# Kernel optimization log

Measured on AMD Instinct MI355X. Metric: run time of the kernel, lower is better.

## Reference

```python
import jax, jax.numpy as jnp
import numpy as np
from math import pi

N = 20000        # nodes
E = 640000       # edges (avg degree 32)
H = 128          # hidden_channels = num_filters
NB = 3           # num_bond_features
NGS = 50 - NB    # gaussians in smearing (num_gaussians - num_bond_features)
CUT = 10.0       # cutoff
L = 3            # num_interactions
B = 16           # graphs in batch
LOG2 = 0.6931471805599453


def ssp(x):
    # ShiftedSoftplus
    return jax.nn.softplus(x) - LOG2


def setup_inputs() -> dict:
    key = jax.random.key(0)
    ks = jax.random.split(key, 20)
    s = 0.05
    inp = {
        "z": jax.random.randint(ks[0], (N,), 0, 100),
        "pos": jax.random.uniform(ks[1], (N, 3), jnp.float32),
        "batch": jnp.sort(jax.random.randint(ks[2], (N,), 0, B)),
        "edge_index": jax.random.randint(ks[3], (2, E), 0, N),
        "edge_attr": jax.random.uniform(ks[4], (E, NB), jnp.float32),
        # parameters (stacked over L interaction blocks where per-layer)
        "emb": jax.random.normal(ks[5], (100, H), jnp.float32) * s,
        "mlp_w1": jax.random.normal(ks[6], (L, NB + NGS, H), jnp.float32) * s,
        "mlp_b1": jnp.zeros((L, H), jnp.float32),
        "mlp_w2": jax.random.normal(ks[7], (L, H, H), jnp.float32) * s,
        "mlp_b2": jnp.zeros((L, H), jnp.float32),
        "cf1_w": jax.random.normal(ks[8], (L, H, H), jnp.float32) * s,   # lin1, no bias
        "cf2_w": jax.random.normal(ks[9], (L, H, H), jnp.float32) * s,
        "cf2_b": jnp.zeros((L, H), jnp.float32),
        "lin_w": jax.random.normal(ks[10], (L, H, H), jnp.float32) * s,
        "lin_b": jnp.zeros((L, H), jnp.float32),
        "out1_w": jax.random.normal(ks[11], (H, H // 2), jnp.float32) * s,
        "out1_b": jnp.zeros((H // 2,), jnp.float32),
        "out2_w": jax.random.normal(ks[12], (H // 2, 1), jnp.float32) * s,
        "out2_b": jnp.zeros((1,), jnp.float32),
    }
    return inp


def reference(z, pos, batch, edge_index, edge_attr, emb,
              mlp_w1, mlp_b1, mlp_w2, mlp_b2,
              cf1_w, cf2_w, cf2_b, lin_w, lin_b,
              out1_w, out1_b, out2_w, out2_b):
    row, col = edge_index[0], edge_index[1]  # source j, target i
    h = emb[z]                               # [N,H] embedding_e(z)
    # edge_weight = ||pos[row] - pos[col]||
    ew = jnp.linalg.norm(pos[row] - pos[col], axis=-1)  # [E]
    # GaussianSmearing(0, cutoff, NGS)
    offset = jnp.linspace(0.0, CUT, NGS, dtype=jnp.float32)
    coeff = -0.5 / (offset[1] - offset[0]) ** 2
    gs = jnp.exp(coeff * (ew[:, None] - offset[None, :]) ** 2)  # [E,NGS]
    ea = jnp.concatenate([edge_attr, gs], axis=1)  # [E,50]
    # cosine cutoff weight
    C = 0.5 * (jnp.cos(ew * pi / CUT) + 1.0)       # [E]
    for l in range(L):
        # filter MLP on edge features
        W = ssp(ea @ mlp_w1[l] + mlp_b1[l]) @ mlp_w2[l] + mlp_b2[l]  # [E,H]
        W = W * C[:, None]
        xh = h @ cf1_w[l]                    # lin1 (no bias) [N,H]
        msg = xh[row] * W                    # gather-mul [E,H]
        agg = jax.ops.segment_sum(msg, col, num_segments=N)  # scatter-add [N,H]
        xc = agg @ cf2_w[l] + cf2_b[l]       # lin2
        xc = ssp(xc)
        xc = xc @ lin_w[l] + lin_b[l]        # block output lin
        h = h + xc                           # residual
    h = ssp(h @ out1_w + out1_b)             # [N,H/2]
    per_node = h @ out2_w + out2_b           # [N,1]
    out = jax.ops.segment_sum(per_node, batch, num_segments=B)  # readout 'add' -> [B,1]
    return out
```

## Files before the change

### kernel.cpp

```cpp
#include <hip/hip_runtime.h>
#include <hip/hip_bf16.h>

typedef __attribute__((ext_vector_type(8))) short bfrag;
typedef __attribute__((ext_vector_type(4))) float f32x4;

__device__ __forceinline__ float ssp_f(float x) {
    return fmaxf(x, 0.f) + __logf(1.f + __expf(-fabsf(x))) - 0.6931471805599453f;
}

__device__ __forceinline__ unsigned short f2b(float x) {
    __hip_bfloat16 h = __float2bfloat16(x);
    return *(unsigned short*)&h;
}

__device__ __forceinline__ unsigned int pk2(float a, float b) {
    __hip_bfloat162 h2 = __float22bfloat162_rn(make_float2(a, b));
    return *(unsigned int*)&h2;
}

__device__ __forceinline__ void stage32x128(
    const float* __restrict__ src, long r0, int N, int t, short (*dst)[136])
{
    #pragma unroll
    for (int j = 0; j < 4; ++j) {
        const int fi = t + j * 256;
        const int r = fi >> 5, c4 = (fi & 31) << 2;
        const long n = r0 + r;
        float4 v = make_float4(0.f, 0.f, 0.f, 0.f);
        if (n < N) v = *(const float4*)(src + n * 128 + c4);
        *(uint2*)&dst[r][c4] = make_uint2(pk2(v.x, v.y), pk2(v.z, v.w));
    }
}

__global__ void sniff_kernel(const unsigned int* __restrict__ raw, int* __restrict__ flag)
{
    __shared__ int cnt[256];
    const int t = threadIdx.x;
    unsigned int w = raw[t];
    unsigned int e = (w >> 7) & 0xFFu;
    cnt[t] = (e >= 100u && e <= 135u) ? 1 : 0;
    __syncthreads();
    for (int s = 128; s > 0; s >>= 1) {
        if (t < s) cnt[t] += cnt[t + s];
        __syncthreads();
    }
    if (t == 0) *flag = (cnt[0] >= 160) ? 1 : 0;
}

__global__ void sniff_int_kernel(const unsigned int* __restrict__ z, int* __restrict__ iflag)
{
    __shared__ int cnt[128];
    const int t = threadIdx.x;
    cnt[t] = (z[2 * t + 1] == 0u) ? 1 : 0;
    __syncthreads();
    for (int s = 64; s > 0; s >>= 1) {
        if (t < s) cnt[t] += cnt[t + s];
        __syncthreads();
    }
    if (t == 0) *iflag = (cnt[0] >= 126) ? 1 : 0;
}

struct Cvt16 {
    const void* src[16];
    long off[17];
};

__global__ __launch_bounds__(256) void convert_fused_kernel(
    Cvt16 args, float* __restrict__ F, long total, const int* __restrict__ flag)
{
    long i = (long)blockIdx.x * 256 + threadIdx.x;
    if (i >= total) return;
    int lo = 0, hi = 16;
    while (hi - lo > 1) {
        int mid = (lo + hi) >> 1;
        if (i >= args.off[mid]) lo = mid; else hi = mid;
    }
    long loc = i - args.off[lo];
    if (*flag) F[i] = __bfloat162float(((const __hip_bfloat16*)args.src[lo])[loc]);
    else       F[i] = ((const float*)args.src[lo])[loc];
}

__global__ __launch_bounds__(256) void convert_int_kernel(
    const void* __restrict__ src, int* __restrict__ dst, int n,
    const int* __restrict__ iflag)
{
    int i = blockIdx.x * 256 + threadIdx.x;
    if (i >= n) return;
    if (*iflag) dst[i] = (int)(((const long long*)src)[i]);
    else        dst[i] = ((const int*)src)[i];
}

__global__ __launch_bounds__(256) void embed_kernel(
    const int* __restrict__ z, const float* __restrict__ embf,
    float* __restrict__ h, int NH)
{
    int idx = blockIdx.x * 256 + threadIdx.x;
    if (idx >= NH) return;
    h[idx] = embf[z[idx >> 7] * 128 + (idx & 127)];
}

__global__ __launch_bounds__(256) void zero_int_kernel(int* p, int n)
{
    int i = blockIdx.x * 256 + threadIdx.x;
    if (i < n) p[i] = 0;
}

__global__ __launch_bounds__(256) void hist_kernel(const int* __restrict__ col,
                                                   int* __restrict__ count, int E)
{
    int e = blockIdx.x * 256 + threadIdx.x;
    if (e < E) atomicAdd(&count[col[e]], 1);
}

__global__ __launch_bounds__(256) void scan_kernel(const int* __restrict__ count,
                                                   int* __restrict__ rowptr,
                                                   int* __restrict__ next, int N)
{
    __shared__ int part[256];
    const int t = threadIdx.x;
    const int chunk = (N + 255) / 256;
    const int lo = t * chunk, hi = min(lo + chunk, N);
    int s = 0;
    for (int i = lo; i < hi; ++i) s += count[i];
    part[t] = s;
    __syncthreads();
    if (t == 0) {
        int run = 0;
        for (int i = 0; i < 256; ++i) { int v = part[i]; part[i] = run; run += v; }
        rowptr[N] = run;
    }
    __syncthreads();
    int run = part[t];
    for (int i = lo; i < hi; ++i) {
        rowptr[i] = run; next[i] = run;
        run += count[i];
    }
}

__global__ __launch_bounds__(256) void prep_scatter_kernel(
    const float* __restrict__ posf, const int* __restrict__ row,
    const int* __restrict__ col, const float* __restrict__ eattrf,
    int* __restrict__ next,
    int* __restrict__ rowS, int* __restrict__ colS,
    float* __restrict__ CS, float* __restrict__ ewS,
    unsigned short* __restrict__ eaS, int E, int NB)
{
    int e = blockIdx.x * 256 + threadIdx.x;
    if (e >= E) return;
    const int r = row[e], c = col[e];
    const int p = atomicAdd(&next[c], 1);
    float dx = posf[r*3+0] - posf[c*3+0];
    float dy = posf[r*3+1] - posf[c*3+1];
    float dz = posf[r*3+2] - posf[c*3+2];
    float ew = sqrtf(dx*dx + dy*dy + dz*dz);
    rowS[p] = r; colS[p] = c; ewS[p] = ew;
    CS[p] = 0.5f * (cosf(ew * 0.3141592653589793f) + 1.0f);
    unsigned short* o = eaS + (long)p * 4;
    for (int q = 0; q < 4; ++q)
        o[q] = (q < NB) ? f2b(eattrf[(long)e * NB + q]) : (unsigned short)0;
}

__global__ __launch_bounds__(256) void wtrans_kernel(
    const float* __restrict__ src, unsigned short* __restrict__ dst,
    int K, int Kpad, int N)
{
    int idx = blockIdx.x * 256 + threadIdx.x;
    if (idx >= N * Kpad) return;
    int n = idx / Kpad, k = idx - n * Kpad;
    dst[idx] = (k < K) ? f2b(src[k * N + n]) : (unsigned short)0;
}

__global__ __launch_bounds__(256) void wtrans_node_kernel(
    const float* __restrict__ cf1, const float* __restrict__ cf2,
    const float* __restrict__ lin, unsigned short* __restrict__ dst, int total)
{
    int idx = blockIdx.x * 256 + threadIdx.x;
    if (idx >= total) return;
    int m = idx >> 14;
    int fam = m % 3, l = m / 3;
    int local = idx & 16383;
    int n = local >> 7, k = local & 127;
    const float* src = (fam == 0 ? cf1 : fam == 1 ? cf2 : lin) + (long)l * 16384;
    dst[idx] = f2b(src[k * 128 + n]);
}

template<int MODE>
__global__ __launch_bounds__(256) void node_gemm_tiled(
    const float* __restrict__ in, const float* __restrict__ W,
    const float* __restrict__ bias, float* __restrict__ out, int N)
{
    __shared__ float in_s[32][128];
    const int t = threadIdx.x;
    const long n0 = (long)blockIdx.x * 32;
    for (int i = t; i < 32 * 128; i += 256) {
        long n = n0 + (i >> 7);
        in_s[i >> 7][i & 127] = (n < N) ? in[n * 128 + (i & 127)] : 0.f;
    }
    __syncthreads();
    const int j = t & 31, sub = t >> 5;
    const int c4 = j * 4, rb = sub * 4;
    float acc[4][4];
    float4 bv = make_float4(0.f, 0.f, 0.f, 0.f);
    if (MODE != 0) bv = *(const float4*)(bias + c4);
    #pragma unroll
    for (int i = 0; i < 4; ++i) { acc[i][0]=bv.x; acc[i][1]=bv.y; acc[i][2]=bv.z; acc[i][3]=bv.w; }
    #pragma unroll 4
    for (int k = 0; k < 128; ++k) {
        const float4 wv = *(const float4*)(W + k * 128 + c4);
        #pragma unroll
        for (int i = 0; i < 4; ++i) {
            const float a = in_s[rb + i][k];
            acc[i][0] += a * wv.x; acc[i][1] += a * wv.y;
            acc[i][2] += a * wv.z; acc[i][3] += a * wv.w;
        }
    }
    #pragma unroll
    for (int i = 0; i < 4; ++i) {
        long n = n0 + rb + i;
        if (n >= N) continue;
        float4 o;
        if (MODE == 1) {
            o.x = ssp_f(acc[i][0]); o.y = ssp_f(acc[i][1]);
            o.z = ssp_f(acc[i][2]); o.w = ssp_f(acc[i][3]);
        } else {
            o.x = acc[i][0]; o.y = acc[i][1]; o.z = acc[i][2]; o.w = acc[i][3];
        }
        if (MODE == 2) {
            float4 p = *(const float4*)(out + n * 128 + c4);
            o.x += p.x; o.y += p.y; o.z += p.z; o.w += p.w;
        }
        *(float4*)(out + n * 128 + c4) = o;
    }
}

__global__ __launch_bounds__(256) void node_gemm1_mfma(
    const float* __restrict__ in, const unsigned short* __restrict__ wt,
    float* __restrict__ out, float* __restrict__ aggz, int N)
{
    __shared__ __align__(16) short a_b[32][136];
    const int t = threadIdx.x;
    const long r0 = (long)blockIdx.x * 32;
    stage32x128(in, r0, N, t, a_b);
    {
        const float4 z = make_float4(0.f, 0.f, 0.f, 0.f);
        #pragma unroll
        for (int j = 0; j < 4; ++j) {
            const int fi = t + j * 256;
            const long n = r0 + (fi >> 5);
            if (n < N) *(float4*)(aggz + n * 128 + ((fi & 31) << 2)) = z;
        }
    }
    __syncthreads();
    const int lane = t & 63, w = t >> 6;
    const int colL = lane & 15, quad = lane >> 4;
    const int rt = (w & 1) * 16 + colL;
    const int nh = (w >> 1) * 64;
    f32x4 acc[4];
    #pragma unroll
    for (int tt = 0; tt < 4; ++tt) acc[tt] = (f32x4){0.f, 0.f, 0.f, 0.f};
    #pragma unroll
    for (int ks = 0; ks < 4; ++ks) {
        const bfrag a = *(const bfrag*)&a_b[rt][ks * 32 + quad * 8];
        #pragma unroll
        for (int tt = 0; tt < 4; ++tt) {
            const bfrag wf = *(const bfrag*)&wt[(long)(nh + tt * 16 + colL) * 128 + ks * 32 + quad * 8];
            acc[tt] = __builtin_amdgcn_mfma_f32_16x16x32_bf16(wf, a, acc[tt], 0, 0, 0);
        }
    }
    const long node = r0 + rt;
    if (node < N) {
        float* orow = out + node * 128;
        #pragma unroll
        for (int tt = 0; tt < 4; ++tt) {
            const int c0 = nh + tt * 16 + quad * 4;
            *(float4*)(orow + c0) = make_float4(acc[tt][0], acc[tt][1], acc[tt][2], acc[tt][3]);
        }
    }
}

__global__ __launch_bounds__(256) void node_gemm23_mfma(
    const float* __restrict__ in,
    const unsigned short* __restrict__ w1t, const float* __restrict__ b1,
    const unsigned short* __restrict__ w2t, const float* __restrict__ b2,
    float* __restrict__ h, int N)
{
    __shared__ __align__(16) short a_b[32][136];
    __shared__ __align__(16) short t_b[32][136];
    const int t = threadIdx.x;
    const long r0 = (long)blockIdx.x * 32;
    stage32x128(in, r0, N, t, a_b);
    __syncthreads();
    const int lane = t & 63, w = t >> 6;
    const int colL = lane & 15, quad = lane >> 4;
    const int rt = (w & 1) * 16 + colL;
    const int nh = (w >> 1) * 64;
    {
        f32x4 acc[4];
        #pragma unroll
        for (int tt = 0; tt < 4; ++tt) acc[tt] = (f32x4){0.f, 0.f, 0.f, 0.f};
        #pragma unroll
        for (int ks = 0; ks < 4; ++ks) {
            const bfrag a = *(const bfrag*)&a_b[rt][ks * 32 + quad * 8];
            #pragma unroll
            for (int tt = 0; tt < 4; ++tt) {
                const bfrag wf = *(const bfrag*)&w1t[(long)(nh + tt * 16 + colL) * 128 + ks * 32 + quad * 8];
                acc[tt] = __builtin_amdgcn_mfma_f32_16x16x32_bf16(wf, a, acc[tt], 0, 0, 0);
            }
        }
        #pragma unroll
        for (int tt = 0; tt < 4; ++tt) {
            const int c0 = nh + tt * 16 + quad * 4;
            const float4 bv = *(const float4*)(b1 + c0);
            const float v0 = ssp_f(acc[tt][0] + bv.x);
            const float v1 = ssp_f(acc[tt][1] + bv.y);
            const float v2 = ssp_f(acc[tt][2] + bv.z);
            const float v3 = ssp_f(acc[tt][3] + bv.w);
            *(uint2*)&t_b[rt][c0] = make_uint2(pk2(v0, v1), pk2(v2, v3));
        }
    }
    __syncthreads();
    {
        f32x4 acc[4];
        #pragma unroll
        for (int tt = 0; tt < 4; ++tt) acc[tt] = (f32x4){0.f, 0.f, 0.f, 0.f};
        #pragma unroll
        for (int ks = 0; ks < 4; ++ks) {
            const bfrag a = *(const bfrag*)&t_b[rt][ks * 32 + quad * 8];
            #pragma unroll
            for (int tt = 0; tt < 4; ++tt) {
                const bfrag wf = *(const bfrag*)&w2t[(long)(nh + tt * 16 + colL) * 128 + ks * 32 + quad * 8];
                acc[tt] = __builtin_amdgcn_mfma_f32_16x16x32_bf16(wf, a, acc[tt], 0, 0, 0);
            }
        }
        const long node = r0 + rt;
        if (node < N) {
            float* hrow = h + node * 128;
            #pragma unroll
            for (int tt = 0; tt < 4; ++tt) {
                const int c0 = nh + tt * 16 + quad * 4;
                const float4 bv = *(const float4*)(b2 + c0);
                float4 hv = *(const float4*)(hrow + c0);
                hv.x += acc[tt][0] + bv.x;
                hv.y += acc[tt][1] + bv.y;
                hv.z += acc[tt][2] + bv.z;
                hv.w += acc[tt][3] + bv.w;
                *(float4*)(hrow + c0) = hv;
            }
        }
    }
}

__global__ __launch_bounds__(256, 8) void edge_mfma(
    const int* __restrict__ rowS, const int* __restrict__ colS,
    const float* __restrict__ CS, const float* __restrict__ ewS,
    const unsigned short* __restrict__ eaS,
    const unsigned short* __restrict__ w1t, const float* __restrict__ b1,
    const unsigned short* __restrict__ w2t, const float* __restrict__ b2,
    const float* __restrict__ xh, float* __restrict__ agg,
    int E, int NB, int F50, float delta, float coeff)
{
    __shared__ __align__(16) char smem[32 * 132 * 4];
    short (*ea_b)[64]    = (short(*)[64])smem;
    short (*t_b)[128]    = (short(*)[128])(smem + 4096);
    float (*runbuf)[132] = (float(*)[132])smem;
    __shared__ int   row_s[32];
    __shared__ int   col_s[32];
    __shared__ float C_s[32];
    __shared__ float ew_s[32];

    const int t = threadIdx.x;
    const long p0 = (long)blockIdx.x * 32;

    if (t < 32) {
        long p = p0 + t; if (p >= E) p = E - 1;
        row_s[t] = rowS[p];
        col_s[t] = colS[p];
        C_s[t]   = (p0 + t < E) ? CS[p] : 0.f;
        ew_s[t]  = ewS[p];
    }
    __syncthreads();
    #pragma unroll
    for (int j = 0; j < 4; ++j) {
        const int pi = t + j * 256;
        const int e  = pi >> 5;
        const int k0 = (pi & 31) * 2;
        long p = p0 + e; if (p >= E) p = E - 1;
        const float ew = ew_s[e];
        float f[2];
        #pragma unroll
        for (int q = 0; q < 2; ++q) {
            const int k = k0 + q;
            if (k < NB) {
                unsigned int ui = (unsigned int)eaS[p * 4 + k] << 16;
                f[q] = *(float*)&ui;
            } else if (k < F50) {
                const float d = ew - (float)(k - NB) * delta;
                f[q] = __expf(coeff * d * d);
            } else f[q] = 0.f;
        }
        *(unsigned int*)&ea_b[e][k0 ^ ((e & 7) << 3)] = pk2(f[0], f[1]);
    }
    __syncthreads();

    const int lane = t & 63;
    const int w    = t >> 6;
    const int colL = lane & 15;
    const int quad = lane >> 4;
    const int et   = (w & 1) * 16 + colL;
    const int nh   = (w >> 1) * 64;
    const int esw  = (et & 7) << 3;
    const float Ct = C_s[et];

    {
        f32x4 acc[4];
        #pragma unroll
        for (int tt = 0; tt < 4; ++tt) acc[tt] = (f32x4){0.f, 0.f, 0.f, 0.f};
        #pragma unroll
        for (int ks = 0; ks < 2; ++ks) {
            const bfrag ea = *(const bfrag*)&ea_b[et][(ks * 32 + quad * 8) ^ esw];
            #pragma unroll
            for (int tt = 0; tt < 4; ++tt) {
                const bfrag wf = *(const bfrag*)&w1t[(long)(nh + tt * 16 + colL) * 64 + ks * 32 + quad * 8];
                acc[tt] = __builtin_amdgcn_mfma_f32_16x16x32_bf16(wf, ea, acc[tt], 0, 0, 0);
            }
        }
        #pragma unroll
        for (int tt = 0; tt < 4; ++tt) {
            const int c0 = nh + tt * 16 + quad * 4;
            const float4 bv = *(const float4*)(b1 + c0);
            const float v0 = ssp_f(acc[tt][0] + bv.x) * Ct;
            const float v1 = ssp_f(acc[tt][1] + bv.y) * Ct;
            const float v2 = ssp_f(acc[tt][2] + bv.z) * Ct;
            const float v3 = ssp_f(acc[tt][3] + bv.w) * Ct;
            *(uint2*)&t_b[et][c0 ^ esw] = make_uint2(pk2(v0, v1), pk2(v2, v3));
        }
    }
    __syncthreads();

    {
        const float* xrow = xh + (long)row_s[et] * 128;
        const float4 xv0 = *(const float4*)(xrow + nh +  0 + quad * 4);
        const float4 xv1 = *(const float4*)(xrow + nh + 16 + quad * 4);
        const float4 xv2 = *(const float4*)(xrow + nh + 32 + quad * 4);
        const float4 xv3 = *(const float4*)(xrow + nh + 48 + quad * 4);
        f32x4 acc[4];
        #pragma unroll
        for (int tt = 0; tt < 4; ++tt) acc[tt] = (f32x4){0.f, 0.f, 0.f, 0.f};
        #pragma unroll
        for (int ks = 0; ks < 4; ++ks) {
            const bfrag tf = *(const bfrag*)&t_b[et][(ks * 32 + quad * 8) ^ esw];
            #pragma unroll
            for (int tt = 0; tt < 4; ++tt) {
                const bfrag wf = *(const bfrag*)&w2t[(long)(nh + tt * 16 + colL) * 128 + ks * 32 + quad * 8];
                acc[tt] = __builtin_amdgcn_mfma_f32_16x16x32_bf16(wf, tf, acc[tt], 0, 0, 0);
            }
        }
        __syncthreads();
        const float4 xv[4] = {xv0, xv1, xv2, xv3};
        #pragma unroll
        for (int tt = 0; tt < 4; ++tt) {
            const int c0 = nh + tt * 16 + quad * 4;
            const float4 bv = *(const float4*)(b2 + c0);
            float4 o;
            o.x = (acc[tt][0] + Ct * bv.x) * xv[tt].x;
            o.y = (acc[tt][1] + Ct * bv.y) * xv[tt].y;
            o.z = (acc[tt][2] + Ct * bv.z) * xv[tt].z;
            o.w = (acc[tt][3] + Ct * bv.w) * xv[tt].w;
            *(float4*)&runbuf[et][c0] = o;
        }
    }
    __syncthreads();

    {
        const int cc   = t & 127;
        const int e0h  = (t >> 7) * 16;
        float a     = runbuf[e0h][cc];
        int  curcol = col_s[e0h];
        #pragma unroll 4
        for (int e = e0h + 1; e < e0h + 16; ++e) {
            const int c2 = col_s[e];
            if (c2 != curcol) {
                atomicAdd(&agg[(long)curcol * 128 + cc], a);
                a = 0.f; curcol = c2;
            }
            a += runbuf[e][cc];
        }
        atomicAdd(&agg[(long)curcol * 128 + cc], a);
    }
}

__global__ __launch_bounds__(256) void edge_atomic(
    const float* __restrict__ posf,
    const int* __restrict__ row, const int* __restrict__ col,
    const float* __restrict__ eattrf,
    const float* __restrict__ w1, const float* __restrict__ b1,
    const float* __restrict__ w2, const float* __restrict__ b2,
    const float* __restrict__ xh, float* __restrict__ agg,
    int E, int NB, int F50, float delta, float coeff)
{
    __shared__ float ea_s[32][52];
    __shared__ float t_s[32][128];
    __shared__ int   row_s[32];
    __shared__ int   col_s[32];
    __shared__ float C_s[32];
    __shared__ float ew_s[32];

    const int t = threadIdx.x;
    const long e0 = (long)blockIdx.x * 32;

    if (t < 32) {
        long e = e0 + t; if (e >= E) e = E - 1;
        const int r = row[e], c = col[e];
        row_s[t] = r; col_s[t] = c;
        float dx = posf[r*3+0] - posf[c*3+0];
        float dy = posf[r*3+1] - posf[c*3+1];
        float dz = posf[r*3+2] - posf[c*3+2];
        float ew = sqrtf(dx*dx + dy*dy + dz*dz);
        ew_s[t] = ew;
        C_s[t]  = (e0 + t < E) ? 0.5f * (cosf(ew * 0.3141592653589793f) + 1.0f) : 0.f;
        for (int q = 0; q < NB; ++q)
            ea_s[t][q] = eattrf[e * NB + q];
    }
    __syncthreads();
    {
        const int NGS = F50 - NB;
        for (int i = t; i < 32 * NGS; i += 256) {
            const int e = i / NGS, g = i - e * NGS;
            const float d = ew_s[e] - (float)g * delta;
            ea_s[e][NB + g] = __expf(coeff * d * d);
        }
    }
    __syncthreads();

    const int j = t & 31, sub = t >> 5;
    const int c4 = j * 4, eb = sub * 4;
    float acc[4][4];
    {
        const float4 bv = *(const float4*)(b1 + c4);
        #pragma unroll
        for (int i = 0; i < 4; ++i) { acc[i][0]=bv.x; acc[i][1]=bv.y; acc[i][2]=bv.z; acc[i][3]=bv.w; }
        for (int k = 0; k < F50; ++k) {
            const float4 wv = *(const float4*)(w1 + k * 128 + c4);
            #pragma unroll
            for (int i = 0; i < 4; ++i) {
                const float a = ea_s[eb + i][k];
                acc[i][0] += a * wv.x; acc[i][1] += a * wv.y;
                acc[i][2] += a * wv.z; acc[i][3] += a * wv.w;
            }
        }
        #pragma unroll
        for (int i = 0; i < 4; ++i) {
            float4 o;
            o.x = ssp_f(acc[i][0]); o.y = ssp_f(acc[i][1]);
            o.z = ssp_f(acc[i][2]); o.w = ssp_f(acc[i][3]);
            *(float4*)&t_s[eb + i][c4] = o;
        }
    }
    __syncthreads();
    {
        const float4 bv = *(const float4*)(b2 + c4);
        #pragma unroll
        for (int i = 0; i < 4; ++i) { acc[i][0]=bv.x; acc[i][1]=bv.y; acc[i][2]=bv.z; acc[i][3]=bv.w; }
        #pragma unroll 4
        for (int k = 0; k < 128; ++k) {
            const float4 wv = *(const float4*)(w2 + k * 128 + c4);
            #pragma unroll
            for (int i = 0; i < 4; ++i) {
                const float a = t_s[eb + i][k];
                acc[i][0] += a * wv.x; acc[i][1] += a * wv.y;
                acc[i][2] += a * wv.z; acc[i][3] += a * wv.w;
            }
        }
    }
    #pragma unroll
    for (int i = 0; i < 4; ++i) {
        const int e = eb + i;
        if (e0 + e >= E) continue;
        const float Ce = C_s[e];
        const float4 xv = *(const float4*)(xh + (long)row_s[e] * 128 + c4);
        float* ag = agg + (long)col_s[e] * 128 + c4;
        atomicAdd(ag + 0, acc[i][0] * Ce * xv.x);
        atomicAdd(ag + 1, acc[i][1] * Ce * xv.y);
        atomicAdd(ag + 2, acc[i][2] * Ce * xv.z);
        atomicAdd(ag + 3, acc[i][3] * Ce * xv.w);
    }
}

__global__ __launch_bounds__(256) void readout_mfma(
    const float* __restrict__ h, const unsigned short* __restrict__ o1t,
    const float* __restrict__ o1b, const float* __restrict__ o2w,
    const float* __restrict__ o2b, const int* __restrict__ batch,
    float* __restrict__ accb, int N)
{
    __shared__ __align__(16) short a_b[32][136];
    __shared__ float nb[32];
    const int t = threadIdx.x;
    const long r0 = (long)blockIdx.x * 32;
    stage32x128(h, r0, N, t, a_b);
    if (t < 32) nb[t] = 0.f;
    __syncthreads();
    const int lane = t & 63, w = t >> 6;
    const int colL = lane & 15, quad = lane >> 4;
    const int rt = (w & 1) * 16 + colL;
    const int nh = (w >> 1) * 32;
    f32x4 acc[2];
    #pragma unroll
    for (int tt = 0; tt < 2; ++tt) acc[tt] = (f32x4){0.f, 0.f, 0.f, 0.f};
    #pragma unroll
    for (int ks = 0; ks < 4; ++ks) {
        const bfrag a = *(const bfrag*)&a_b[rt][ks * 32 + quad * 8];
        #pragma unroll
        for (int tt = 0; tt < 2; ++tt) {
            const bfrag wf = *(const bfrag*)&o1t[(long)(nh + tt * 16 + colL) * 128 + ks * 32 + quad * 8];
            acc[tt] = __builtin_amdgcn_mfma_f32_16x16x32_bf16(wf, a, acc[tt], 0, 0, 0);
        }
    }
    float s = 0.f;
    #pragma unroll
    for (int tt = 0; tt < 2; ++tt) {
        const int c0 = nh + tt * 16 + quad * 4;
        const float4 bv = *(const float4*)(o1b + c0);
        const float4 wv = *(const float4*)(o2w + c0);
        s += ssp_f(acc[tt][0] + bv.x) * wv.x;
        s += ssp_f(acc[tt][1] + bv.y) * wv.y;
        s += ssp_f(acc[tt][2] + bv.z) * wv.z;
        s += ssp_f(acc[tt][3] + bv.w) * wv.w;
    }
    s += __shfl_xor(s, 16);
    s += __shfl_xor(s, 32);
    if (quad == 0) atomicAdd(&nb[rt], s);
    __syncthreads();
    if (t < 32) {
        const long node = r0 + t;
        if (node < N) atomicAdd(&accb[batch[node]], nb[t] + o2b[0]);
    }
}

__global__ __launch_bounds__(128) void readout_simple(
    const float* __restrict__ h,
    const float* __restrict__ o1w, const float* __restrict__ o1b,
    const float* __restrict__ o2w, const float* __restrict__ o2b,
    const int* __restrict__ batch, float* __restrict__ accb)
{
    __shared__ float hr[128];
    __shared__ float vv[64];
    const int n = blockIdx.x;
    const int t = threadIdx.x;
    hr[t] = h[(long)n * 128 + t];
    __syncthreads();
    if (t < 64) {
        float a = o1b[t];
        #pragma unroll 8
        for (int k = 0; k < 128; ++k)
            a = fmaf(hr[k], o1w[k * 64 + t], a);
        vv[t] = ssp_f(a) * o2w[t];
    }
    __syncthreads();
    if (t < 32) vv[t] += vv[t + 32];
    __syncthreads();
    if (t < 16) vv[t] += vv[t + 16];
    __syncthreads();
    if (t < 8)  vv[t] += vv[t + 8];
    __syncthreads();
    if (t < 4)  vv[t] += vv[t + 4];
    __syncthreads();
    if (t < 2)  vv[t] += vv[t + 2];
    __syncthreads();
    if (t == 0) atomicAdd(&accb[batch[n]], vv[0] + vv[1] + o2b[0]);
}

__global__ void finalize_kernel(const float* __restrict__ accb,
                                float* __restrict__ out, int B)
{
    int t = blockIdx.x * 256 + threadIdx.x;
    if (t < B) out[t] = accb[t];
}

extern "C" void kernel_launch(void* const* d_in, const int* in_sizes, int n_in,
                              void* d_out, int out_size, void* d_ws, size_t ws_size,
                              hipStream_t stream)
{
    const int N   = in_sizes[0];
    const int E   = in_sizes[3] / 2;
    const int B   = out_size;
    const int H   = 128;
    const int L   = in_sizes[7] / H;
    const int NB  = in_sizes[4] / E;
    const int F50 = in_sizes[6] / (L * H);
    const int NGS = F50 - NB;
    const float delta = 10.0f / (float)(NGS - 1);
    const float coeff = -0.5f / (delta * delta);

    const int fidx[16] = {1, 4, 5, 6, 7, 8, 9, 10, 11, 12, 13, 14, 15, 16, 17, 18};
    Cvt16 cv;
    cv.off[0] = 0;
    for (int i = 0; i < 16; ++i) {
        cv.src[i] = d_in[fidx[i]];
        cv.off[i + 1] = cv.off[i] + in_sizes[fidx[i]];
    }
    const long ftot = cv.off[16];

    float* F = (float*)d_ws;
    long base = (ftot + 3) & ~3L;
    float* h    = F + base;
    float* xh   = h + (long)N * H;
    float* agg  = xh + (long)N * H;
    float* accb = agg + (long)N * H;
    int*   flag  = (int*)(accb + ((B + 3) & ~3));
    int*   iflag = flag + 1;
    int*   zi     = flag + 4;
    int*   batchi = zi + N;
    int*   eidxi  = batchi + N;
    int*   count  = eidxi + 2 * E;
    int*   rowptr = count + N;
    int*   next   = rowptr + N + 1;
    int*   rowS   = next + N;
    int*   colS   = rowS + E;
    float* CS     = (float*)(colS + E);
    float* ewS    = CS + E;
    unsigned short* eaS = (unsigned short*)(ewS + E);
    unsigned short* w1t = eaS + 4L * E;
    unsigned short* w2t = w1t + (long)L * 128 * 64;
    unsigned short* nwt = w2t + (long)L * 128 * 128;
    unsigned short* o1t = nwt + 3L * L * 128 * 128;
    long used_bytes = (long)((char*)(o1t + 64 * 128) - (char*)d_ws);
    const bool use_fast = (used_bytes <= (long)ws_size) && (F50 <= 64) && (NB <= 4);

    sniff_kernel<<<1, 256, 0, stream>>>((const unsigned int*)d_in[5], flag);
    sniff_int_kernel<<<1, 128, 0, stream>>>((const unsigned int*)d_in[0], iflag);

    convert_fused_kernel<<<(int)((ftot + 255) / 256), 256, 0, stream>>>(cv, F, ftot, flag);
    convert_int_kernel<<<(N + 255) / 256, 256, 0, stream>>>(d_in[0], zi, N, iflag);
    convert_int_kernel<<<(N + 255) / 256, 256, 0, stream>>>(d_in[2], batchi, N, iflag);
    convert_int_kernel<<<(2 * E + 255) / 256, 256, 0, stream>>>(d_in[3], eidxi, 2 * E, iflag);

    const float* posf   = F + cv.off[0];
    const float* eattrf = F + cv.off[1];
    const float* embf   = F + cv.off[2];
    const float* w1   = F + cv.off[3];  const float* b1   = F + cv.off[4];
    const float* w2   = F + cv.off[5];  const float* b2   = F + cv.off[6];
    const float* cf1  = F + cv.off[7];  const float* cf2  = F + cv.off[8];
    const float* cf2b = F + cv.off[9];  const float* lin  = F + cv.off[10];
    const float* linb = F + cv.off[11]; const float* o1   = F + cv.off[12];
    const float* o1b  = F + cv.off[13]; const float* o2   = F + cv.off[14];
    const float* o2b  = F + cv.off[15];

    if (use_fast) {
        zero_int_kernel<<<(N + 255) / 256, 256, 0, stream>>>(count, N);
        hist_kernel<<<(E + 255) / 256, 256, 0, stream>>>(eidxi + E, count, E);
        scan_kernel<<<1, 256, 0, stream>>>(count, rowptr, next, N);
        prep_scatter_kernel<<<(E + 255) / 256, 256, 0, stream>>>(
            posf, eidxi, eidxi + E, eattrf, next, rowS, colS, CS, ewS, eaS, E, NB);
        for (int l = 0; l < L; ++l) {
            wtrans_kernel<<<(128 * 64 + 255) / 256, 256, 0, stream>>>(
                w1 + (long)l * F50 * H, w1t + (long)l * 128 * 64, F50, 64, 128);
            wtrans_kernel<<<(128 * 128 + 255) / 256, 256, 0, stream>>>(
                w2 + (long)l * H * H, w2t + (long)l * 128 * 128, 128, 128, 128);
        }
        const int ntot = 3 * L * 128 * 128;
        wtrans_node_kernel<<<(ntot + 255) / 256, 256, 0, stream>>>(cf1, cf2, lin, nwt, ntot);
        wtrans_kernel<<<(64 * 128 + 255) / 256, 256, 0, stream>>>(o1, o1t, 128, 128, 64);
    }

    embed_kernel<<<(N * H + 255) / 256, 256, 0, stream>>>(zi, embf, h, N * H);
    hipMemsetAsync(accb, 0, (size_t)B * sizeof(float), stream);

    const int ngemm = (N + 31) / 32;
    const int nedge = (E + 31) / 32;
    for (int l = 0; l < L; ++l) {
        if (use_fast) {
            node_gemm1_mfma<<<ngemm, 256, 0, stream>>>(
                h, nwt + (long)(l * 3 + 0) * 16384, xh, agg, N);
            edge_mfma<<<nedge, 256, 0, stream>>>(
                rowS, colS, CS, ewS, eaS,
                w1t + (long)l * 128 * 64, b1 + (long)l * H,
                w2t + (long)l * 128 * 128, b2 + (long)l * H,
                xh, agg, E, NB, F50, delta, coeff);
            node_gemm23_mfma<<<ngemm, 256, 0, stream>>>(
                agg, nwt + (long)(l * 3 + 1) * 16384, cf2b + (long)l * H,
                nwt + (long)(l * 3 + 2) * 16384, linb + (long)l * H, h, N);
        } else {
            hipMemsetAsync(agg, 0, (size_t)N * H * sizeof(float), stream);
            node_gemm_tiled<0><<<ngemm, 256, 0, stream>>>(h, cf1 + (long)l * H * H, nullptr, xh, N);
            edge_atomic<<<nedge, 256, 0, stream>>>(
                posf, eidxi, eidxi + E, eattrf,
                w1 + (long)l * F50 * H, b1 + (long)l * H,
                w2 + (long)l * H * H,  b2 + (long)l * H,
                xh, agg, E, NB, F50, delta, coeff);
            node_gemm_tiled<1><<<ngemm, 256, 0, stream>>>(agg, cf2 + (long)l * H * H, cf2b + (long)l * H, xh, N);
            node_gemm_tiled<2><<<ngemm, 256, 0, stream>>>(xh, lin + (long)l * H * H, linb + (long)l * H, h, N);
        }
    }

    if (use_fast) {
        readout_mfma<<<ngemm, 256, 0, stream>>>(h, o1t, o1b, o2, o2b, batchi, accb, N);
    } else {
        readout_simple<<<N, 128, 0, stream>>>(h, o1, o1b, o2, o2b, batchi, accb);
    }
    finalize_kernel<<<(B + 255) / 256, 256, 0, stream>>>(accb, (float*)d_out, B);
}
```

Baseline: 1.475 ms.

## Precompute bf16 edge features once and swap MFMA operand orientation in edge kernel

The prep kernel now writes a 64-wide bf16 edge feature row (bond attributes plus Gaussian smearing) per sorted edge into workspace. The edge kernel reads these rows straight from global memory as MFMA A operands instead of recomputing exponentials and staging through LDS in each of the three layers. The MFMA operands are also swapped so edges form the row dimension: outputs are written transposed into a padded LDS tile, and the cutoff factor C moves from the first-layer activation to the final multiply. This trades repeated exp work and one barrier for extra global traffic of 128 bytes per edge per layer and scalar strided LDS stores.

```diff
diff --git a/kernel.cpp b/kernel.cpp
--- a/kernel.cpp
+++ b/kernel.cpp
@@ -143,7 +143,8 @@
     int* __restrict__ next,
     int* __restrict__ rowS, int* __restrict__ colS,
     float* __restrict__ CS, float* __restrict__ ewS,
-    unsigned short* __restrict__ eaS, int E, int NB)
+    unsigned short* __restrict__ eaS, unsigned short* __restrict__ gs64,
+    int E, int NB, int F50, float delta, float coeff)
 {
     int e = blockIdx.x * 256 + threadIdx.x;
     if (e >= E) return;
@@ -158,6 +159,23 @@
     unsigned short* o = eaS + (long)p * 4;
     for (int q = 0; q < 4; ++q)
         o[q] = (q < NB) ? f2b(eattrf[(long)e * NB + q]) : (unsigned short)0;
+    if (gs64) {
+        unsigned short* g = gs64 + (long)p * 64;
+        #pragma unroll 4
+        for (int k0 = 0; k0 < 64; k0 += 2) {
+            float f[2];
+            #pragma unroll
+            for (int q = 0; q < 2; ++q) {
+                const int k = k0 + q;
+                if (k < NB)        f[q] = eattrf[(long)e * NB + k];
+                else if (k < F50) {
+                    const float d = ew - (float)(k - NB) * delta;
+                    f[q] = __expf(coeff * d * d);
+                } else             f[q] = 0.f;
+            }
+            *(unsigned int*)(g + k0) = pk2(f[0], f[1]);
+        }
+    }
 }
 
 __global__ __launch_bounds__(256) void wtrans_kernel(
@@ -350,18 +368,19 @@
     }
 }
 
+template<int PRE>
 __global__ __launch_bounds__(256, 8) void edge_mfma(
     const int* __restrict__ rowS, const int* __restrict__ colS,
     const float* __restrict__ CS, const float* __restrict__ ewS,
-    const unsigned short* __restrict__ eaS,
+    const unsigned short* __restrict__ eaS, const unsigned short* __restrict__ gs64,
     const unsigned short* __restrict__ w1t, const float* __restrict__ b1,
     const unsigned short* __restrict__ w2t, const float* __restrict__ b2,
     const float* __restrict__ xh, float* __restrict__ agg,
     int E, int NB, int F50, float delta, float coeff)
 {
     __shared__ __align__(16) char smem[32 * 132 * 4];
-    short (*ea_b)[64]    = (short(*)[64])smem;
-    short (*t_b)[128]    = (short(*)[128])(smem + 4096);
+    short (*t_b)[136]    = (short(*)[136])smem;
+    short (*ea_b)[64]    = (short(*)[64])(smem + 8704);
     float (*runbuf)[132] = (float(*)[132])smem;
     __shared__ int   row_s[32];
     __shared__ int   col_s[32];
@@ -376,97 +395,108 @@
         row_s[t] = rowS[p];
         col_s[t] = colS[p];
         C_s[t]   = (p0 + t < E) ? CS[p] : 0.f;
-        ew_s[t]  = ewS[p];
-    }
-    __syncthreads();
-    #pragma unroll
-    for (int j = 0; j < 4; ++j) {
-        const int pi = t + j * 256;
-        const int e  = pi >> 5;
-        const int k0 = (pi & 31) * 2;
-        long p = p0 + e; if (p >= E) p = E - 1;
-        const float ew = ew_s[e];
-        float f[2];
-        #pragma unroll
-        for (int q = 0; q < 2; ++q) {
-            const int k = k0 + q;
-            if (k < NB) {
-                unsigned int ui = (unsigned int)eaS[p * 4 + k] << 16;
-                f[q] = *(float*)&ui;
-            } else if (k < F50) {
-                const float d = ew - (float)(k - NB) * delta;
-                f[q] = __expf(coeff * d * d);
-            } else f[q] = 0.f;
-        }
-        *(unsigned int*)&ea_b[e][k0 ^ ((e & 7) << 3)] = pk2(f[0], f[1]);
-    }
-    __syncthreads();
+        if (!PRE) ew_s[t] = ewS[p];
+    }
+    __syncthreads();
+    if (!PRE) {
+        #pragma unroll
+        for (int j = 0; j < 4; ++j) {
+            const int pi = t + j * 256;
+            const int e  = pi >> 5;
+            const int k0 = (pi & 31) * 2;
+            long p = p0 + e; if (p >= E) p = E - 1;
+            const float ew = ew_s[e];
+            float f[2];
+            #pragma unroll
+            for (int q = 0; q < 2; ++q) {
+                const int k = k0 + q;
+                if (k < NB) {
+                    unsigned int ui = (unsigned int)eaS[p * 4 + k] << 16;
+                    f[q] = *(float*)&ui;
+                } else if (k < F50) {
+                    const float d = ew - (float)(k - NB) * delta;
+                    f[q] = __expf(coeff * d * d);
+                } else f[q] = 0.f;
+            }
+            *(unsigned int*)&ea_b[e][k0 ^ ((e & 7) << 3)] = pk2(f[0], f[1]);
+        }
+        __syncthreads();
+    }
 
     const int lane = t & 63;
     const int w    = t >> 6;
     const int colL = lane & 15;
     const int quad = lane >> 4;
-    const int et   = (w & 1) * 16 + colL;
-    const int nh   = (w >> 1) * 64;
-    const int esw  = (et & 7) << 3;
-    const float Ct = C_s[et];
+    const int m0   = (w & 1) * 16;
+    const int ar   = m0 + colL;
 
     {
         f32x4 acc[4];
         #pragma unroll
         for (int tt = 0; tt < 4; ++tt) acc[tt] = (f32x4){0.f, 0.f, 0.f, 0.f};
+        const unsigned short* earow = nullptr;
+        if (PRE) {
+            long p = p0 + ar; if (p >= E) p = E - 1;
+            earow = gs64 + p * 64;
+        }
+        const int asw = (ar & 7) << 3;
         #pragma unroll
         for (int ks = 0; ks < 2; ++ks) {
-            const bfrag ea = *(const bfrag*)&ea_b[et][(ks * 32 + quad * 8) ^ esw];
+            bfrag a;
+            if (PRE) a = *(const bfrag*)&earow[ks * 32 + quad * 8];
+            else     a = *(const bfrag*)&ea_b[ar][(ks * 32 + quad * 8) ^ asw];
             #pragma unroll
             for (int tt = 0; tt < 4; ++tt) {
-                const bfrag wf = *(const bfrag*)&w1t[(long)(nh + tt * 16 + colL) * 64 + ks * 32 + quad * 8];
-                acc[tt] = __builtin_amdgcn_mfma_f32_16x16x32_bf16(wf, ea, acc[tt], 0, 0, 0);
+                const int n0 = ((w >> 1) * 4 + tt) * 16;
+                const bfrag b = *(const bfrag*)&w1t[(long)(n0 + colL) * 64 + ks * 32 + quad * 8];
+                acc[tt] = __builtin_amdgcn_mfma_f32_16x16x32_bf16(a, b, acc[tt], 0, 0, 0);
             }
         }
         #pragma unroll
         for (int tt = 0; tt < 4; ++tt) {
-            const int c0 = nh + tt * 16 + quad * 4;
-            const float4 bv = *(const float4*)(b1 + c0);
-            const float v0 = ssp_f(acc[tt][0] + bv.x) * Ct;
-            const float v1 = ssp_f(acc[tt][1] + bv.y) * Ct;
-            const float v2 = ssp_f(acc[tt][2] + bv.z) * Ct;
-            const float v3 = ssp_f(acc[tt][3] + bv.w) * Ct;
-            *(uint2*)&t_b[et][c0 ^ esw] = make_uint2(pk2(v0, v1), pk2(v2, v3));
+            const int n0 = ((w >> 1) * 4 + tt) * 16;
+            const float bcol = b1[n0 + colL];
+            #pragma unroll
+            for (int reg = 0; reg < 4; ++reg)
+                t_b[m0 + quad * 4 + reg][n0 + colL] = (short)f2b(ssp_f(acc[tt][reg] + bcol));
         }
     }
     __syncthreads();
 
     {
-        const float* xrow = xh + (long)row_s[et] * 128;
-        const float4 xv0 = *(const float4*)(xrow + nh +  0 + quad * 4);
-        const float4 xv1 = *(const float4*)(xrow + nh + 16 + quad * 4);
-        const float4 xv2 = *(const float4*)(xrow + nh + 32 + quad * 4);
-        const float4 xv3 = *(const float4*)(xrow + nh + 48 + quad * 4);
+        const int ebase = m0 + quad * 4;
+        float xv[4][4];
+        #pragma unroll
+        for (int reg = 0; reg < 4; ++reg) {
+            const float* xrow = xh + (long)row_s[ebase + reg] * 128;
+            #pragma unroll
+            for (int tt = 0; tt < 4; ++tt)
+                xv[reg][tt] = xrow[((w >> 1) * 4 + tt) * 16 + colL];
+        }
         f32x4 acc[4];
         #pragma unroll
         for (int tt = 0; tt < 4; ++tt) acc[tt] = (f32x4){0.f, 0.f, 0.f, 0.f};
         #pragma unroll
         for (int ks = 0; ks < 4; ++ks) {
-            const bfrag tf = *(const bfrag*)&t_b[et][(ks * 32 + quad * 8) ^ esw];
+            const bfrag a = *(const bfrag*)&t_b[ar][ks * 32 + quad * 8];
             #pragma unroll
             for (int tt = 0; tt < 4; ++tt) {
-                const bfrag wf = *(const bfrag*)&w2t[(long)(nh + tt * 16 + colL) * 128 + ks * 32 + quad * 8];
-                acc[tt] = __builtin_amdgcn_mfma_f32_16x16x32_bf16(wf, tf, acc[tt], 0, 0, 0);
+                const int n0 = ((w >> 1) * 4 + tt) * 16;
+                const bfrag b = *(const bfrag*)&w2t[(long)(n0 + colL) * 128 + ks * 32 + quad * 8];
+                acc[tt] = __builtin_amdgcn_mfma_f32_16x16x32_bf16(a, b, acc[tt], 0, 0, 0);
             }
         }
         __syncthreads();
-        const float4 xv[4] = {xv0, xv1, xv2, xv3};
         #pragma unroll
         for (int tt = 0; tt < 4; ++tt) {
-            const int c0 = nh + tt * 16 + quad * 4;
-            const float4 bv = *(const float4*)(b2 + c0);
-            float4 o;
-            o.x = (acc[tt][0] + Ct * bv.x) * xv[tt].x;
-            o.y = (acc[tt][1] + Ct * bv.y) * xv[tt].y;
-            o.z = (acc[tt][2] + Ct * bv.z) * xv[tt].z;
-            o.w = (acc[tt][3] + Ct * bv.w) * xv[tt].w;
-            *(float4*)&runbuf[et][c0] = o;
+            const int n0 = ((w >> 1) * 4 + tt) * 16;
+            const int cg = n0 + colL;
+            const float bcol = b2[cg];
+            #pragma unroll
+            for (int reg = 0; reg < 4; ++reg) {
+                const int e = ebase + reg;
+                runbuf[e][cg] = (acc[tt][reg] + bcol) * C_s[e] * xv[reg][tt];
+            }
         }
     }
     __syncthreads();
@@ -723,8 +753,11 @@
     unsigned short* w2t = w1t + (long)L * 128 * 64;
     unsigned short* nwt = w2t + (long)L * 128 * 128;
     unsigned short* o1t = nwt + 3L * L * 128 * 128;
+    unsigned short* gs64 = (unsigned short*)(((uintptr_t)(o1t + 64 * 128) + 15) & ~(uintptr_t)15);
     long used_bytes = (long)((char*)(o1t + 64 * 128) - (char*)d_ws);
+    long used_pre   = (long)((char*)(gs64 + 64L * E) - (char*)d_ws);
     const bool use_fast = (used_bytes <= (long)ws_size) && (F50 <= 64) && (NB <= 4);
+    const bool use_pre  = use_fast && (used_pre <= (long)ws_size);
 
     sniff_kernel<<<1, 256, 0, stream>>>((const unsigned int*)d_in[5], flag);
     sniff_int_kernel<<<1, 128, 0, stream>>>((const unsigned int*)d_in[0], iflag);
@@ -750,7 +783,8 @@
         hist_kernel<<<(E + 255) / 256, 256, 0, stream>>>(eidxi + E, count, E);
         scan_kernel<<<1, 256, 0, stream>>>(count, rowptr, next, N);
         prep_scatter_kernel<<<(E + 255) / 256, 256, 0, stream>>>(
-            posf, eidxi, eidxi + E, eattrf, next, rowS, colS, CS, ewS, eaS, E, NB);
+            posf, eidxi, eidxi + E, eattrf, next, rowS, colS, CS, ewS, eaS,
+            use_pre ? gs64 : (unsigned short*)nullptr, E, NB, F50, delta, coeff);
         for (int l = 0; l < L; ++l) {
             wtrans_kernel<<<(128 * 64 + 255) / 256, 256, 0, stream>>>(
                 w1 + (long)l * F50 * H, w1t + (long)l * 128 * 64, F50, 64, 128);
@@ -771,11 +805,18 @@
         if (use_fast) {
             node_gemm1_mfma<<<ngemm, 256, 0, stream>>>(
                 h, nwt + (long)(l * 3 + 0) * 16384, xh, agg, N);
-            edge_mfma<<<nedge, 256, 0, stream>>>(
-                rowS, colS, CS, ewS, eaS,
-                w1t + (long)l * 128 * 64, b1 + (long)l * H,
-                w2t + (long)l * 128 * 128, b2 + (long)l * H,
-                xh, agg, E, NB, F50, delta, coeff);
+            if (use_pre)
+                edge_mfma<1><<<nedge, 256, 0, stream>>>(
+                    rowS, colS, CS, ewS, eaS, gs64,
+                    w1t + (long)l * 128 * 64, b1 + (long)l * H,
+                    w2t + (long)l * 128 * 128, b2 + (long)l * H,
+                    xh, agg, E, NB, F50, delta, coeff);
+            else
+                edge_mfma<0><<<nedge, 256, 0, stream>>>(
+                    rowS, colS, CS, ewS, eaS, gs64,
+                    w1t + (long)l * 128 * 64, b1 + (long)l * H,
+                    w2t + (long)l * 128 * 128, b2 + (long)l * H,
+                    xh, agg, E, NB, F50, delta, coeff);
             node_gemm23_mfma<<<ngemm, 256, 0, stream>>>(
                 agg, nwt + (long)(l * 3 + 1) * 16384, cf2b + (long)l * H,
                 nwt + (long)(l * 3 + 2) * 16384, linb + (long)l * H, h, N);
```

Measured after the change: 1.703 ms. +15.5%, slower.

## Fuse next-layer lin1 into node GEMM and transpose edge MFMA operand layout

Applied to the files above, without the earlier changes.

The lin2/lin node kernel now also computes the next layer's lin1 product from the freshly updated h kept in LDS, writes xh, and zeroes agg. This removes one node-GEMM launch per layer and the extra global reread of h. The edge kernel swaps MFMA operands so each lane holds edge rows rather than feature columns. It applies the cosine cutoff and the xh gather as per-element scalar work in the epilogue instead of scaling before the second GEMM. It also stages the edge features one element at a time, which adds scalar LDS stores and scattered gathers that may cost more than they save.

```diff
diff --git a/kernel.cpp b/kernel.cpp
--- a/kernel.cpp
+++ b/kernel.cpp
@@ -278,11 +278,14 @@
     }
 }
 
+template<int CHAIN>
 __global__ __launch_bounds__(256) void node_gemm23_mfma(
     const float* __restrict__ in,
     const unsigned short* __restrict__ w1t, const float* __restrict__ b1,
     const unsigned short* __restrict__ w2t, const float* __restrict__ b2,
-    float* __restrict__ h, int N)
+    float* __restrict__ h,
+    const unsigned short* __restrict__ cf1t, float* __restrict__ xh,
+    float* __restrict__ aggz, int N)
 {
     __shared__ __align__(16) short a_b[32][136];
     __shared__ __align__(16) short t_b[32][136];
@@ -345,6 +348,35 @@
                 hv.z += acc[tt][2] + bv.z;
                 hv.w += acc[tt][3] + bv.w;
                 *(float4*)(hrow + c0) = hv;
+                if (CHAIN)
+                    *(uint2*)&a_b[rt][c0] = make_uint2(pk2(hv.x, hv.y), pk2(hv.z, hv.w));
+            }
+        }
+    }
+    if (CHAIN) {
+        __syncthreads();
+        f32x4 acc[4];
+        #pragma unroll
+        for (int tt = 0; tt < 4; ++tt) acc[tt] = (f32x4){0.f, 0.f, 0.f, 0.f};
+        #pragma unroll
+        for (int ks = 0; ks < 4; ++ks) {
+            const bfrag a = *(const bfrag*)&a_b[rt][ks * 32 + quad * 8];
+            #pragma unroll
+            for (int tt = 0; tt < 4; ++tt) {
+                const bfrag wf = *(const bfrag*)&cf1t[(long)(nh + tt * 16 + colL) * 128 + ks * 32 + quad * 8];
+                acc[tt] = __builtin_amdgcn_mfma_f32_16x16x32_bf16(wf, a, acc[tt], 0, 0, 0);
+            }
+        }
+        const long node = r0 + rt;
+        if (node < N) {
+            float* orow = xh + node * 128;
+            float* zrow = aggz + node * 128;
+            const float4 z = make_float4(0.f, 0.f, 0.f, 0.f);
+            #pragma unroll
+            for (int tt = 0; tt < 4; ++tt) {
+                const int c0 = nh + tt * 16 + quad * 4;
+                *(float4*)(orow + c0) = make_float4(acc[tt][0], acc[tt][1], acc[tt][2], acc[tt][3]);
+                *(float4*)(zrow + c0) = z;
             }
         }
     }
@@ -379,26 +411,16 @@
         ew_s[t]  = ewS[p];
     }
     __syncthreads();
-    #pragma unroll
-    for (int j = 0; j < 4; ++j) {
-        const int pi = t + j * 256;
-        const int e  = pi >> 5;
-        const int k0 = (pi & 31) * 2;
+    for (int i = t; i < 32 * 64; i += 256) {
+        const int e = i >> 6, k = i & 63;
         long p = p0 + e; if (p >= E) p = E - 1;
-        const float ew = ew_s[e];
-        float f[2];
-        #pragma unroll
-        for (int q = 0; q < 2; ++q) {
-            const int k = k0 + q;
-            if (k < NB) {
-                unsigned int ui = (unsigned int)eaS[p * 4 + k] << 16;
-                f[q] = *(float*)&ui;
-            } else if (k < F50) {
-                const float d = ew - (float)(k - NB) * delta;
-                f[q] = __expf(coeff * d * d);
-            } else f[q] = 0.f;
-        }
-        *(unsigned int*)&ea_b[e][k0 ^ ((e & 7) << 3)] = pk2(f[0], f[1]);
+        unsigned short v;
+        if (k < NB)        v = eaS[p * 4 + k];
+        else if (k < F50) {
+            float d = ew_s[e] - (float)(k - NB) * delta;
+            v = f2b(__expf(coeff * d * d));
+        } else             v = 0;
+        ea_b[e][k ^ ((e & 7) << 3)] = (short)v;
     }
     __syncthreads();
 
@@ -406,67 +428,67 @@
     const int w    = t >> 6;
     const int colL = lane & 15;
     const int quad = lane >> 4;
-    const int et   = (w & 1) * 16 + colL;
-    const int nh   = (w >> 1) * 64;
-    const int esw  = (et & 7) << 3;
-    const float Ct = C_s[et];
+    const int m0   = (w & 1) * 16;
 
     {
         f32x4 acc[4];
         #pragma unroll
         for (int tt = 0; tt < 4; ++tt) acc[tt] = (f32x4){0.f, 0.f, 0.f, 0.f};
+        const int ar  = m0 + colL;
+        const int asw = (ar & 7) << 3;
         #pragma unroll
         for (int ks = 0; ks < 2; ++ks) {
-            const bfrag ea = *(const bfrag*)&ea_b[et][(ks * 32 + quad * 8) ^ esw];
+            const bfrag a = *(const bfrag*)&ea_b[ar][(ks * 32 + quad * 8) ^ asw];
             #pragma unroll
             for (int tt = 0; tt < 4; ++tt) {
-                const bfrag wf = *(const bfrag*)&w1t[(long)(nh + tt * 16 + colL) * 64 + ks * 32 + quad * 8];
-                acc[tt] = __builtin_amdgcn_mfma_f32_16x16x32_bf16(wf, ea, acc[tt], 0, 0, 0);
+                const int n0 = ((w >> 1) * 4 + tt) * 16;
+                const bfrag b = *(const bfrag*)&w1t[(long)(n0 + colL) * 64 + ks * 32 + quad * 8];
+                acc[tt] = __builtin_amdgcn_mfma_f32_16x16x32_bf16(a, b, acc[tt], 0, 0, 0);
             }
         }
         #pragma unroll
         for (int tt = 0; tt < 4; ++tt) {
-            const int c0 = nh + tt * 16 + quad * 4;
-            const float4 bv = *(const float4*)(b1 + c0);
-            const float v0 = ssp_f(acc[tt][0] + bv.x) * Ct;
-            const float v1 = ssp_f(acc[tt][1] + bv.y) * Ct;
-            const float v2 = ssp_f(acc[tt][2] + bv.z) * Ct;
-            const float v3 = ssp_f(acc[tt][3] + bv.w) * Ct;
-            *(uint2*)&t_b[et][c0 ^ esw] = make_uint2(pk2(v0, v1), pk2(v2, v3));
+            const int n0 = ((w >> 1) * 4 + tt) * 16;
+            const float bcol = b1[n0 + colL];
+            #pragma unroll
+            for (int reg = 0; reg < 4; ++reg) {
+                const int rr = m0 + quad * 4 + reg;
+                float v = ssp_f(acc[tt][reg] + bcol);
+                t_b[rr][(n0 + colL) ^ ((rr & 7) << 3)] = (short)f2b(v);
+            }
         }
     }
     __syncthreads();
 
     {
-        const float* xrow = xh + (long)row_s[et] * 128;
-        const float4 xv0 = *(const float4*)(xrow + nh +  0 + quad * 4);
-        const float4 xv1 = *(const float4*)(xrow + nh + 16 + quad * 4);
-        const float4 xv2 = *(const float4*)(xrow + nh + 32 + quad * 4);
-        const float4 xv3 = *(const float4*)(xrow + nh + 48 + quad * 4);
         f32x4 acc[4];
         #pragma unroll
         for (int tt = 0; tt < 4; ++tt) acc[tt] = (f32x4){0.f, 0.f, 0.f, 0.f};
+        const int ar  = m0 + colL;
+        const int asw = (ar & 7) << 3;
         #pragma unroll
         for (int ks = 0; ks < 4; ++ks) {
-            const bfrag tf = *(const bfrag*)&t_b[et][(ks * 32 + quad * 8) ^ esw];
+            const bfrag a = *(const bfrag*)&t_b[ar][(ks * 32 + quad * 8) ^ asw];
             #pragma unroll
             for (int tt = 0; tt < 4; ++tt) {
-                const bfrag wf = *(const bfrag*)&w2t[(long)(nh + tt * 16 + colL) * 128 + ks * 32 + quad * 8];
-                acc[tt] = __builtin_amdgcn_mfma_f32_16x16x32_bf16(wf, tf, acc[tt], 0, 0, 0);
+                const int n0 = ((w >> 1) * 4 + tt) * 16;
+                const bfrag b = *(const bfrag*)&w2t[(long)(n0 + colL) * 128 + ks * 32 + quad * 8];
+                acc[tt] = __builtin_amdgcn_mfma_f32_16x16x32_bf16(a, b, acc[tt], 0, 0, 0);
             }
         }
         __syncthreads();
-        const float4 xv[4] = {xv0, xv1, xv2, xv3};
+        const int ebase = m0 + quad * 4;
         #pragma unroll
         for (int tt = 0; tt < 4; ++tt) {
-            const int c0 = nh + tt * 16 + quad * 4;
-            const float4 bv = *(const float4*)(b2 + c0);
-            float4 o;
-            o.x = (acc[tt][0] + Ct * bv.x) * xv[tt].x;
-            o.y = (acc[tt][1] + Ct * bv.y) * xv[tt].y;
-            o.z = (acc[tt][2] + Ct * bv.z) * xv[tt].z;
-            o.w = (acc[tt][3] + Ct * bv.w) * xv[tt].w;
-            *(float4*)&runbuf[et][c0] = o;
+            const int n0 = ((w >> 1) * 4 + tt) * 16;
+            const int cg = n0 + colL;
+            const float bcol = b2[cg];
+            #pragma unroll
+            for (int reg = 0; reg < 4; ++reg) {
+                const int e = ebase + reg;
+                const float v = acc[tt][reg] + bcol;
+                runbuf[e][cg] = v * C_s[e] * xh[(long)row_s[e] * 128 + cg];
+            }
         }
     }
     __syncthreads();
@@ -767,19 +789,30 @@
 
     const int ngemm = (N + 31) / 32;
     const int nedge = (E + 31) / 32;
-    for (int l = 0; l < L; ++l) {
-        if (use_fast) {
-            node_gemm1_mfma<<<ngemm, 256, 0, stream>>>(
-                h, nwt + (long)(l * 3 + 0) * 16384, xh, agg, N);
+    if (use_fast) {
+        node_gemm1_mfma<<<ngemm, 256, 0, stream>>>(
+            h, nwt + 0, xh, agg, N);
+        for (int l = 0; l < L; ++l) {
             edge_mfma<<<nedge, 256, 0, stream>>>(
                 rowS, colS, CS, ewS, eaS,
                 w1t + (long)l * 128 * 64, b1 + (long)l * H,
                 w2t + (long)l * 128 * 128, b2 + (long)l * H,
                 xh, agg, E, NB, F50, delta, coeff);
-            node_gemm23_mfma<<<ngemm, 256, 0, stream>>>(
-                agg, nwt + (long)(l * 3 + 1) * 16384, cf2b + (long)l * H,
-                nwt + (long)(l * 3 + 2) * 16384, linb + (long)l * H, h, N);
-        } else {
+            if (l < L - 1) {
+                node_gemm23_mfma<1><<<ngemm, 256, 0, stream>>>(
+                    agg, nwt + (long)(l * 3 + 1) * 16384, cf2b + (long)l * H,
+                    nwt + (long)(l * 3 + 2) * 16384, linb + (long)l * H, h,
+                    nwt + (long)((l + 1) * 3 + 0) * 16384, xh, agg, N);
+            } else {
+                node_gemm23_mfma<0><<<ngemm, 256, 0, stream>>>(
+                    agg, nwt + (long)(l * 3 + 1) * 16384, cf2b + (long)l * H,
+                    nwt + (long)(l * 3 + 2) * 16384, linb + (long)l * H, h,
+                    nullptr, nullptr, nullptr, N);
+            }
+        }
+        readout_mfma<<<ngemm, 256, 0, stream>>>(h, o1t, o1b, o2, o2b, batchi, accb, N);
+    } else {
+        for (int l = 0; l < L; ++l) {
             hipMemsetAsync(agg, 0, (size_t)N * H * sizeof(float), stream);
             node_gemm_tiled<0><<<ngemm, 256, 0, stream>>>(h, cf1 + (long)l * H * H, nullptr, xh, N);
             edge_atomic<<<nedge, 256, 0, stream>>>(
@@ -790,11 +823,6 @@
             node_gemm_tiled<1><<<ngemm, 256, 0, stream>>>(agg, cf2 + (long)l * H * H, cf2b + (long)l * H, xh, N);
             node_gemm_tiled<2><<<ngemm, 256, 0, stream>>>(xh, lin + (long)l * H * H, linb + (long)l * H, h, N);
         }
-    }
-
-    if (use_fast) {
-        readout_mfma<<<ngemm, 256, 0, stream>>>(h, o1t, o1b, o2, o2b, batchi, accb, N);
-    } else {
         readout_simple<<<N, 128, 0, stream>>>(h, o1, o1b, o2, o2b, batchi, accb);
     }
     finalize_kernel<<<(B + 255) / 256, 256, 0, stream>>>(accb, (float*)d_out, B);
```

New measurement: 1.367 ms. -7.3%, faster.
